# Kernel tuning notes

Measured on AMD Instinct MI355X. Metric: run time of the kernel, lower is better.

Reference implementation:

```python
import jax, jax.numpy as jnp
import numpy as np
from jax import lax

TOP_K = 8
N_EXPERTS = 256
N_GROUP = 8
TOPK_GROUP = 4
ROUTED_SCALING = 2.5
NORM_TOPK_PROB = True


def setup_inputs() -> dict:
    key = jax.random.key(0)
    k1, k2, k3 = jax.random.split(key, 3)
    hidden_states = jax.random.normal(k1, (4, 4096, 4096), dtype=jnp.float32)
    weight = jax.random.normal(k2, (N_EXPERTS, 4096), dtype=jnp.float32) * 0.02
    e_score_correction_bias = jax.random.normal(k3, (N_EXPERTS,), dtype=jnp.float32) * 0.1
    return {
        "hidden_states": hidden_states,
        "weight": weight,
        "e_score_correction_bias": e_score_correction_bias,
    }


def reference(hidden_states, weight, e_score_correction_bias):
    bsz, seq_len, h = hidden_states.shape
    T = bsz * seq_len
    x = hidden_states.reshape(T, h).astype(jnp.float32)
    # gate GEMM: [T, h] x [E, h]^T -> [T, E]
    logits = jnp.einsum("th,eh->te", x, weight.astype(jnp.float32))
    scores = jax.nn.sigmoid(logits)

    scores_for_choice = scores + e_score_correction_bias[None, :]  # [T, E]
    eg = N_EXPERTS // N_GROUP  # experts per group
    grp = scores_for_choice.reshape(T, N_GROUP, eg)
    top2, _ = lax.top_k(grp, 2)                      # [T, G, 2]
    group_scores = top2.sum(axis=-1)                  # [T, G]
    _, group_idx = lax.top_k(group_scores, TOPK_GROUP)  # [T, topk_group]
    group_mask = jnp.zeros((T, N_GROUP), dtype=scores.dtype)
    group_mask = group_mask.at[jnp.arange(T)[:, None], group_idx].set(1.0)
    score_mask = jnp.broadcast_to(group_mask[:, :, None], (T, N_GROUP, eg)).reshape(T, N_EXPERTS)

    neg_inf = jnp.float32(-jnp.inf)
    tmp_scores = jnp.where(score_mask > 0, scores_for_choice, neg_inf)
    _, topk_idx = lax.top_k(tmp_scores, TOP_K)        # [T, top_k]
    topk_weight = jnp.take_along_axis(scores, topk_idx, axis=1)

    if TOP_K > 1 and NORM_TOPK_PROB:
        denom = topk_weight.sum(axis=-1, keepdims=True) + 1e-20
        topk_weight = topk_weight / denom
    topk_weight = topk_weight * ROUTED_SCALING
    return topk_idx, topk_weight
```

## Files before the change

kernel.cpp:

```cpp
#include <hip/hip_runtime.h>
#include <math.h>

#define Hdim 4096
#define NE 256
#define BM 32
#define BK 32
#define NKC (Hdim / BK)
#define PLANE_ELEMS (Hdim * NE)
#define CHUNK_ELEMS 8192

#define C0 9.765625e-4f
#define C1 4.76837158203125e-7f

typedef _Float16 f16x8 __attribute__((ext_vector_type(8)));
typedef _Float16 f16x4 __attribute__((ext_vector_type(4)));
typedef float f32x4 __attribute__((ext_vector_type(4)));

__global__ __launch_bounds__(256)
void convert_w(const float* __restrict__ W, _Float16* __restrict__ pl) {
  const int id = blockIdx.x * 256 + threadIdx.x;
  const int k8 = id & 511;
  const int n = id >> 9;
  const float* src = W + (long)n * Hdim + k8 * 8;
  const float4 x0 = *(const float4*)src;
  const float4 x1 = *(const float4*)(src + 4);
  const float xv[8] = {x0.x, x0.y, x0.z, x0.w, x1.x, x1.y, x1.z, x1.w};
  f16x8 vh, vm;
#pragma unroll
  for (int j = 0; j < 8; ++j) {
    const float v = xv[j] * 64.f;
    const _Float16 h = (_Float16)v;
    const float r = (v - (float)h) * 2048.f;
    vh[j] = h;
    vm[j] = (_Float16)r;
  }
  const long co = ((long)k8 * NE + n) * 8;
  *(f16x8*)(pl + co) = vh;
  *(f16x8*)(pl + PLANE_ELEMS + co) = vm;
}

__global__ __launch_bounds__(512, 4)
void moe_gate_fused(const float* __restrict__ X, const _Float16* __restrict__ pl,
                    const float* __restrict__ bias, float* __restrict__ out, int T) {
  __shared__ __align__(16) unsigned char smem[36864];
  const int tid = threadIdx.x;
  const int lane = tid & 63, wave = tid >> 6;
  const int r16 = lane & 15, c4 = lane >> 4;
  const long bm0 = (long)blockIdx.x * BM;

  f32x4 acc0[2][2], acc1[2][2];
#pragma unroll
  for (int i = 0; i < 2; ++i)
#pragma unroll
    for (int j = 0; j < 2; ++j) {
      acc0[i][j] = (f32x4)(0.f);
      acc1[i][j] = (f32x4)(0.f);
    }

  const int xm = tid >> 3;
  const int xf = tid & 7;
  const float* xsrc = X + (bm0 + xm) * (long)Hdim + xf * 4;
  const int xws = ((xf >> 1) * 32 + xm) * 16 + (xf & 1) * 8;

  const _Float16* wsrc0 = pl + ((size_t)(c4 * 256 + wave * 32 + r16)) * 8;
  const _Float16* wsrc1 = wsrc0 + PLANE_ELEMS;

  f16x8 wA[2][2], wB[2][2];

#define LOADW(dst, kc_)                                                         \
  {                                                                             \
    const size_t ko = (size_t)(kc_) * CHUNK_ELEMS;                              \
    _Pragma("unroll") for (int fn = 0; fn < 2; ++fn) {                          \
      dst[0][fn] = *(const f16x8*)(wsrc0 + ko + fn * 128);                      \
      dst[1][fn] = *(const f16x8*)(wsrc1 + ko + fn * 128);                      \
    }                                                                           \
  }

#define WRITE_X(b, xr)                                                          \
  if (tid < 256) {                                                              \
    f16x4 vh, vm;                                                               \
    const float xa[4] = {(xr).x, (xr).y, (xr).z, (xr).w};                       \
    _Pragma("unroll") for (int j = 0; j < 4; ++j) {                             \
      const float v = xa[j] * 16.f;                                             \
      const _Float16 h = (_Float16)v;                                           \
      const float r = (v - (float)h) * 2048.f;                                  \
      vh[j] = h;                                                                \
      vm[j] = (_Float16)r;                                                      \
    }                                                                           \
    const int xo = (b) * 4096;                                                  \
    *(f16x4*)&smem[xo + 0 * 2048 + xws] = vh;                                   \
    *(f16x4*)&smem[xo + 1 * 2048 + xws] = vm;                                   \
  }

#define COMPUTE(b, wreg)                                                        \
  {                                                                             \
    const int xo = (b) * 4096;                                                  \
    f16x8 af[2][2];                                                             \
    _Pragma("unroll") for (int p = 0; p < 2; ++p)                               \
        _Pragma("unroll") for (int fm = 0; fm < 2; ++fm)                        \
            af[p][fm] = *(const f16x8*)&smem[xo + p * 2048 +                    \
                                             (c4 * 32 + fm * 16 + r16) * 16];   \
    _Pragma("unroll") for (int fm = 0; fm < 2; ++fm)                            \
        _Pragma("unroll") for (int fn = 0; fn < 2; ++fn) {                      \
      acc0[fm][fn] = __builtin_amdgcn_mfma_f32_16x16x32_f16(                    \
          af[0][fm], wreg[0][fn], acc0[fm][fn], 0, 0, 0);                       \
      f32x4 s = acc1[fm][fn];                                                   \
      s = __builtin_amdgcn_mfma_f32_16x16x32_f16(af[0][fm], wreg[1][fn], s, 0, 0, 0); \
      s = __builtin_amdgcn_mfma_f32_16x16x32_f16(af[1][fm], wreg[0][fn], s, 0, 0, 0); \
      acc1[fm][fn] = s;                                                         \
    }                                                                           \
  }

  {
    const float4 x0 = (tid < 256) ? *(const float4*)(xsrc)
                                  : make_float4(0.f, 0.f, 0.f, 0.f);
    WRITE_X(0, x0);
  }
  LOADW(wA, 0);
  __syncthreads();

  for (int kc = 0; kc < NKC; kc += 2) {
    {
      float4 xn = make_float4(0.f, 0.f, 0.f, 0.f);
      if (tid < 256) xn = *(const float4*)(xsrc + (size_t)(kc + 1) * BK);
      LOADW(wB, kc + 1);
      COMPUTE(0, wA);
      WRITE_X(1, xn);
      __syncthreads();
    }
    {
      const int k2 = (kc + 2 < NKC) ? kc + 2 : NKC - 1;
      float4 xn = make_float4(0.f, 0.f, 0.f, 0.f);
      if (tid < 256) xn = *(const float4*)(xsrc + (size_t)k2 * BK);
      LOADW(wA, k2);
      COMPUTE(1, wB);
      if (kc + 2 < NKC) WRITE_X(0, xn);
      __syncthreads();
    }
  }

  float* lg = (float*)smem;
#pragma unroll
  for (int fm = 0; fm < 2; ++fm)
#pragma unroll
    for (int fn = 0; fn < 2; ++fn)
#pragma unroll
      for (int r = 0; r < 4; ++r) {
        const int t = fm * 16 + c4 * 4 + r;
        const int n = wave * 32 + fn * 16 + r16;
        lg[t * 260 + n] = fmaf(acc1[fm][fn][r], C1, acc0[fm][fn][r] * C0);
      }
  __syncthreads();

  const float4 bv = *(const float4*)(bias + lane * 4);
  for (int i = 0; i < 4; ++i) {
    const int t = wave * 4 + i;
    const float4 lgv = *(const float4*)&lg[t * 260 + lane * 4];

    const float s0 = 1.f / (1.f + expf(-lgv.x));
    const float s1 = 1.f / (1.f + expf(-lgv.y));
    const float s2 = 1.f / (1.f + expf(-lgv.z));
    const float s3 = 1.f / (1.f + expf(-lgv.w));

    const float c0 = s0 + bv.x, c1 = s1 + bv.y, c2 = s2 + bv.z, c3 = s3 + bv.w;

    float m1 = fmaxf(c0, c1), m2 = fminf(c0, c1);
    if (c2 > m1) { m2 = m1; m1 = c2; } else m2 = fmaxf(m2, c2);
    if (c3 > m1) { m2 = m1; m1 = c3; } else m2 = fmaxf(m2, c3);
#pragma unroll
    for (int off = 1; off < 8; off <<= 1) {
      const float o1 = __shfl_xor(m1, off);
      const float o2 = __shfl_xor(m2, off);
      if (o1 > m1) { m2 = fmaxf(m1, o2); m1 = o1; }
      else m2 = fmaxf(m2, o1);
    }
    const float gs = m1 + m2;

    const int gme = lane >> 3;
    int rank = 0;
#pragma unroll
    for (int j = 0; j < 8; ++j) {
      const float gj = __shfl(gs, j * 8);
      rank += ((gj > gs) || (gj == gs && j < gme)) ? 1 : 0;
    }
    const bool sel = rank < 4;

    const float NEG = -INFINITY;
    float q0 = sel ? c0 : NEG, q1 = sel ? c1 : NEG;
    float q2 = sel ? c2 : NEG, q3 = sel ? c3 : NEG;

    float sum = 0.f;
    int my_e = 0;
    float my_w = 0.f;
#pragma unroll
    for (int r = 0; r < 8; ++r) {
      float v = q0; int ix = 0;
      if (q1 > v) { v = q1; ix = 1; }
      if (q2 > v) { v = q2; ix = 2; }
      if (q3 > v) { v = q3; ix = 3; }
      int e = lane * 4 + ix;
#pragma unroll
      for (int off = 1; off < 64; off <<= 1) {
        const float v2 = __shfl_xor(v, off);
        const int e2 = __shfl_xor(e, off);
        const bool take = (v2 > v) || (v2 == v && e2 < e);
        v = take ? v2 : v;
        e = take ? e2 : e;
      }
      const int slot = e & 3, owner = e >> 2;
      const float svs = (slot == 0) ? s0 : ((slot == 1) ? s1 : ((slot == 2) ? s2 : s3));
      const float wgt = __shfl(svs, owner);
      sum += wgt;
      if (lane == r) { my_e = e; my_w = wgt; }
      const bool own = (lane == owner);
      q0 = (own && slot == 0) ? NEG : q0;
      q1 = (own && slot == 1) ? NEG : q1;
      q2 = (own && slot == 2) ? NEG : q2;
      q3 = (own && slot == 3) ? NEG : q3;
    }

    if (lane < 8) {
      const float denom = sum + 1e-20f;
      const long tg = bm0 + t;
      out[tg * 8 + lane] = (float)my_e;
      out[(long)T * 8 + tg * 8 + lane] = my_w / denom * 2.5f;
    }
  }
}

extern "C" void kernel_launch(void* const* d_in, const int* in_sizes, int n_in,
                              void* d_out, int out_size, void* d_ws, size_t ws_size,
                              hipStream_t stream) {
  const float* X = (const float*)d_in[0];
  const float* W = (const float*)d_in[1];
  const float* B = (const float*)d_in[2];
  float* out = (float*)d_out;
  const int T = in_sizes[0] / Hdim;

  _Float16* planes = (_Float16*)d_ws;

  convert_w<<<512, 256, 0, stream>>>(W, planes);
  moe_gate_fused<<<T / BM, 512, 0, stream>>>(X, planes, B, out, T);
}
```

Before: 170.9 us.

## Process two K-chunks per barrier stage using all 512 threads for X staging

The main loop now covers 64 K-elements per pipeline stage instead of 32, so there are half as many __syncthreads barriers. All 512 threads load and convert X instead of only 256. Two extra weight register sets (wC, wD) are added so that two chunks of W stay in flight while the current pair is computed. The shared buffer per stage doubles within the existing 36 KB allocation. The cost is higher register pressure, which may hurt occupancy under the 512x4 launch bounds.

```diff
diff --git a/kernel.cpp b/kernel.cpp
--- a/kernel.cpp
+++ b/kernel.cpp
@@ -57,15 +57,16 @@
       acc1[i][j] = (f32x4)(0.f);
     }
 
-  const int xm = tid >> 3;
-  const int xf = tid & 7;
+  const int xm = tid >> 4;
+  const int xf = tid & 15;
   const float* xsrc = X + (bm0 + xm) * (long)Hdim + xf * 4;
-  const int xws = ((xf >> 1) * 32 + xm) * 16 + (xf & 1) * 8;
+  const int xws = (xf >> 3) * 4096 +
+                  (((xf & 7) >> 1) * 32 + xm) * 16 + (xf & 1) * 8;
 
   const _Float16* wsrc0 = pl + ((size_t)(c4 * 256 + wave * 32 + r16)) * 8;
   const _Float16* wsrc1 = wsrc0 + PLANE_ELEMS;
 
-  f16x8 wA[2][2], wB[2][2];
+  f16x8 wA[2][2], wB[2][2], wC[2][2], wD[2][2];
 
 #define LOADW(dst, kc_)                                                         \
   {                                                                             \
@@ -76,8 +77,8 @@
     }                                                                           \
   }
 
-#define WRITE_X(b, xr)                                                          \
-  if (tid < 256) {                                                              \
+#define WRITE_X2(b, xr)                                                         \
+  {                                                                             \
     f16x4 vh, vm;                                                               \
     const float xa[4] = {(xr).x, (xr).y, (xr).z, (xr).w};                       \
     _Pragma("unroll") for (int j = 0; j < 4; ++j) {                             \
@@ -87,14 +88,14 @@
       vh[j] = h;                                                                \
       vm[j] = (_Float16)r;                                                      \
     }                                                                           \
-    const int xo = (b) * 4096;                                                  \
-    *(f16x4*)&smem[xo + 0 * 2048 + xws] = vh;                                   \
-    *(f16x4*)&smem[xo + 1 * 2048 + xws] = vm;                                   \
-  }
-
-#define COMPUTE(b, wreg)                                                        \
+    const int xo = (b) * 8192 + xws;                                            \
+    *(f16x4*)&smem[xo] = vh;                                                    \
+    *(f16x4*)&smem[xo + 2048] = vm;                                             \
+  }
+
+#define COMPUTE(b, sc, wreg)                                                    \
   {                                                                             \
-    const int xo = (b) * 4096;                                                  \
+    const int xo = (b) * 8192 + (sc) * 4096;                                    \
     f16x8 af[2][2];                                                             \
     _Pragma("unroll") for (int p = 0; p < 2; ++p)                               \
         _Pragma("unroll") for (int fm = 0; fm < 2; ++fm)                        \
@@ -112,29 +113,31 @@
   }
 
   {
-    const float4 x0 = (tid < 256) ? *(const float4*)(xsrc)
-                                  : make_float4(0.f, 0.f, 0.f, 0.f);
-    WRITE_X(0, x0);
+    const float4 x0 = *(const float4*)(xsrc);
+    WRITE_X2(0, x0);
   }
   LOADW(wA, 0);
+  LOADW(wB, 1);
   __syncthreads();
 
-  for (int kc = 0; kc < NKC; kc += 2) {
+  for (int p = 0; p < NKC / 2; p += 2) {
     {
-      float4 xn = make_float4(0.f, 0.f, 0.f, 0.f);
-      if (tid < 256) xn = *(const float4*)(xsrc + (size_t)(kc + 1) * BK);
-      LOADW(wB, kc + 1);
-      COMPUTE(0, wA);
-      WRITE_X(1, xn);
+      const float4 xn = *(const float4*)(xsrc + (size_t)(p + 1) * 64);
+      LOADW(wC, 2 * p + 2);
+      LOADW(wD, 2 * p + 3);
+      COMPUTE(0, 0, wA);
+      COMPUTE(0, 1, wB);
+      WRITE_X2(1, xn);
       __syncthreads();
     }
     {
-      const int k2 = (kc + 2 < NKC) ? kc + 2 : NKC - 1;
-      float4 xn = make_float4(0.f, 0.f, 0.f, 0.f);
-      if (tid < 256) xn = *(const float4*)(xsrc + (size_t)k2 * BK);
-      LOADW(wA, k2);
-      COMPUTE(1, wB);
-      if (kc + 2 < NKC) WRITE_X(0, xn);
+      const int pn = (p + 2 < NKC / 2) ? p + 2 : NKC / 2 - 1;
+      const float4 xn = *(const float4*)(xsrc + (size_t)pn * 64);
+      LOADW(wA, 2 * pn);
+      LOADW(wB, 2 * pn + 1);
+      COMPUTE(1, 0, wC);
+      COMPUTE(1, 1, wD);
+      if (p + 2 < NKC / 2) WRITE_X2(0, xn);
       __syncthreads();
     }
   }
```

After: 165.1 us. 1.04x faster.
